# Performance work log

Measured on AMD Instinct MI355X. Metric: run time of the kernel, lower is better.

The kernel has to match this reference:

```python
import jax, jax.numpy as jnp
import numpy as np

B, IN_C, OUT_C, K, Z_DIM = 32, 128, 128, 3, 512
H, W, STRIDE = 56, 56, 1


def setup_inputs() -> dict:
    key = jax.random.key(0)
    k1, k2, k3 = jax.random.split(key, 3)
    x = jax.random.normal(k1, (B, IN_C, H, W), dtype=jnp.float32)
    z = jax.random.normal(k2, (B, Z_DIM), dtype=jnp.float32)
    # nn.Linear(z_dim, out_c*in_c*k*k): weight [out_f, in_f], bias [out_f]
    out_f = OUT_C * IN_C * K * K
    W_head = jax.random.normal(k3, (out_f, Z_DIM), dtype=jnp.float32) * (1.0 / np.sqrt(Z_DIM))
    b_head = jnp.zeros((out_f,), dtype=jnp.float32)
    return {"x": x, "z": z, "W_head": W_head, "b_head": b_head}


def reference(x, z, W_head, b_head):
    b = x.shape[0]
    # hypernetwork head: per-sample conv weights
    w = z @ W_head.T + b_head                       # [B, out_c*in_c*k*k]
    w = w.reshape(b, OUT_C, IN_C, K, K)             # [B, O, I, K, K]

    pad = K // 2

    def conv_one(xi, wi):
        # xi: [I, H, W], wi: [O, I, K, K] -> [O, H', W']
        out = jax.lax.conv_general_dilated(
            xi[None],                                # [1, I, H, W]
            wi,
            window_strides=(STRIDE, STRIDE),
            padding=[(pad, pad), (pad, pad)],
            dimension_numbers=("NCHW", "OIHW", "NCHW"),
        )
        return out[0]

    return jax.vmap(conv_one)(x, w)                 # [B, O, H', W']
```

## Files before the change

### kernel.cpp

```cpp
#include <hip/hip_runtime.h>
#include <hip/hip_bf16.h>
#include <stdint.h>

#define BB 32
#define IC 128
#define OC 128
#define HH 56
#define WW 56
#define ZD 512
#define NRS 9
#define OI (OC*IC)
#define WROWS (OI*NRS)
#define WDIM 58

typedef float  f32x4  __attribute__((ext_vector_type(4)));
typedef short  bf16x8 __attribute__((ext_vector_type(8)));

static __device__ __forceinline__ short f2bf(float f) {
    uint32_t u = __float_as_uint(f);
    uint32_t r = (u + 0x7fffu + ((u >> 16) & 1u)) >> 16;
    return (short)r;
}
static __device__ __forceinline__ short f2bf_hw(float f) {
    __hip_bfloat16 h = __float2bfloat16(f);
    return *reinterpret_cast<short*>(&h);
}

__global__ __launch_bounds__(256) void head_kernel(
    const float* __restrict__ Wh, const float* __restrict__ z,
    const float* __restrict__ bh, short* __restrict__ wout)
{
    __shared__ __align__(16) char Zl[32 * 1024];
    const int tid = threadIdx.x;

    {
        const int b = tid >> 3, ks = (tid & 7) * 64;
        const float* zp = z + (size_t)b * ZD + ks;
        const int bx = (b & 7) << 4;
        #pragma unroll
        for (int j8 = 0; j8 < 8; ++j8) {
            f32x4 v0 = *(const f32x4*)(zp + j8 * 8);
            f32x4 v1 = *(const f32x4*)(zp + j8 * 8 + 4);
            bf16x8 pk;
            pk[0] = f2bf_hw(v0.x); pk[1] = f2bf_hw(v0.y);
            pk[2] = f2bf_hw(v0.z); pk[3] = f2bf_hw(v0.w);
            pk[4] = f2bf_hw(v1.x); pk[5] = f2bf_hw(v1.y);
            pk[6] = f2bf_hw(v1.z); pk[7] = f2bf_hw(v1.w);
            *(bf16x8*)(Zl + b * 1024 + ((ks * 2 + j8 * 16) ^ bx)) = pk;
        }
    }
    __syncthreads();

    const int lane = tid & 63;
    const int wv   = tid >> 6;
    const int rl   = lane & 15;
    const int kq   = lane >> 4;
    const int rowg = blockIdx.x * 64 + wv * 16 + rl;
    const float* wp = Wh + (size_t)rowg * ZD + kq * 8;
    const int zxor = (rl & 7) << 4;

    f32x4 acc0 = {0.f, 0.f, 0.f, 0.f}, acc1 = {0.f, 0.f, 0.f, 0.f};
    #pragma unroll 4
    for (int kb = 0; kb < 16; ++kb) {
        f32x4 w0 = *(const f32x4*)(wp + kb * 32);
        f32x4 w1 = *(const f32x4*)(wp + kb * 32 + 4);
        bf16x8 bw;
        bw[0] = f2bf_hw(w0.x); bw[1] = f2bf_hw(w0.y);
        bw[2] = f2bf_hw(w0.z); bw[3] = f2bf_hw(w0.w);
        bw[4] = f2bf_hw(w1.x); bw[5] = f2bf_hw(w1.y);
        bw[6] = f2bf_hw(w1.z); bw[7] = f2bf_hw(w1.w);
        const int koff = (kb * 64 + kq * 16) ^ zxor;
        bf16x8 a0 = *(const bf16x8*)(Zl + rl * 1024 + koff);
        bf16x8 a1 = *(const bf16x8*)(Zl + (16 + rl) * 1024 + koff);
        acc0 = __builtin_amdgcn_mfma_f32_16x16x32_bf16(a0, bw, acc0, 0, 0, 0);
        acc1 = __builtin_amdgcn_mfma_f32_16x16x32_bf16(a1, bw, acc1, 0, 0, 0);
    }

    const float bias = bh[rowg];
    const int oi = rowg / 9, rs = rowg - oi * 9;
    const size_t outb = (size_t)rs * OI + oi;
    #pragma unroll
    for (int r = 0; r < 4; ++r) {
        const int b0 = kq * 4 + r;
        wout[(size_t)b0 * WROWS + outb]        = f2bf(acc0[r] + bias);
        wout[(size_t)(16 + b0) * WROWS + outb] = f2bf(acc1[r] + bias);
    }
}

__global__ __launch_bounds__(256) void transpose_kernel(
    const float* __restrict__ x, short* __restrict__ xt)
{
    const int h = blockIdx.x;
    const int b = blockIdx.y;
    const int w = threadIdx.x & 63;
    const int yq = threadIdx.x >> 6;
    if (w >= WW) return;
    const float* xp = x + (size_t)b * IC * HH * WW + h * WW + w;
    short* op = xt + (((size_t)(b * HH + h)) * WW + w) * IC;
    #pragma unroll
    for (int q = 0; q < 4; ++q) {
        int ic = yq * 4 + q;
        bf16x8 pk;
        #pragma unroll
        for (int j = 0; j < 8; ++j) {
            float v = xp[(size_t)(ic * 8 + j) * (HH * WW)];
            pk[j] = f2bf(v);
        }
        *(bf16x8*)(op + ic * 8) = pk;
    }
}

__global__ __launch_bounds__(256) void conv_kernel(
    const short* __restrict__ wbf,
    const short* __restrict__ xt,
    float* __restrict__ out)
{
    __shared__ __align__(16) char Xl[3 * WDIM * 256];
    __shared__ __align__(16) char Wl[128 * 256];
    const int tid  = threadIdx.x;
    const int lane = tid & 63;
    const int wv   = tid >> 6;
    const int h = blockIdx.x;
    const int b = blockIdx.y;

    #pragma unroll
    for (int q = 0; q < 11; ++q) {
        int idx = tid + q * 256;
        if (idx < 3 * WDIM * 16) ((f32x4*)Xl)[idx] = (f32x4){0.f, 0.f, 0.f, 0.f};
    }
    __syncthreads();

    for (int r = 0; r < 3; ++r) {
        int hin = h + r - 1;
        if (hin < 0 || hin >= HH) continue;
        const char* src = (const char*)(xt + ((size_t)(b * HH + hin)) * WW * IC);
        char* dstbase = Xl + (r * WDIM + 1) * 256;
        for (int it = wv; it < 14; it += 4) {
            int c = it * 64 + lane;
            int u = r * WDIM + 1 + (c >> 4);
            int soff = (c * 16) ^ ((u & 7) << 4);
            __builtin_amdgcn_global_load_lds(
                (const __attribute__((address_space(1))) uint32_t*)(src + soff),
                (__attribute__((address_space(3))) uint32_t*)(dstbase + it * 1024),
                16, 0, 0);
        }
    }

    f32x4 acc[2][4];
    #pragma unroll
    for (int a = 0; a < 2; ++a)
        #pragma unroll
        for (int p = 0; p < 4; ++p) acc[a][p] = (f32x4){0.f, 0.f, 0.f, 0.f};

    const int axor = (lane & 7) << 4;
    int kkoff[4];
    #pragma unroll
    for (int kk = 0; kk < 4; ++kk) kkoff[kk] = kk * 64 + ((lane >> 4) << 4);

    for (int rs = 0; rs < 9; ++rs) {
        __syncthreads();
        const char* wsrc = (const char*)(wbf + ((size_t)b * NRS + rs) * OI);
        for (int it = wv; it < 32; it += 4) {
            int c = it * 64 + lane;
            int soff = (c * 16) ^ (((c >> 4) & 7) << 4);
            __builtin_amdgcn_global_load_lds(
                (const __attribute__((address_space(1))) uint32_t*)(wsrc + soff),
                (__attribute__((address_space(3))) uint32_t*)(Wl + it * 1024),
                16, 0, 0);
        }
        __syncthreads();

        const int r = rs / 3, s = rs - 3 * (rs / 3);
        int ubase[4], bswz[4];
        #pragma unroll
        for (int pf = 0; pf < 4; ++pf) {
            int p = pf * 16 + (lane & 15);
            int pc = p > 55 ? 55 : p;
            int uu = r * WDIM + pc + s;
            ubase[pf] = uu * 256;
            bswz[pf] = (uu & 7) << 4;
        }
        #pragma unroll
        for (int kk = 0; kk < 4; ++kk) {
            bf16x8 a0 = *(const bf16x8*)(Wl + (wv * 32 + (lane & 15)) * 256 +
                                         (kkoff[kk] ^ axor));
            bf16x8 a1 = *(const bf16x8*)(Wl + (wv * 32 + 16 + (lane & 15)) * 256 +
                                         (kkoff[kk] ^ axor));
            #pragma unroll
            for (int pf = 0; pf < 4; ++pf) {
                bf16x8 bv = *(const bf16x8*)(Xl + ubase[pf] + (kkoff[kk] ^ bswz[pf]));
                acc[0][pf] = __builtin_amdgcn_mfma_f32_16x16x32_bf16(a0, bv, acc[0][pf], 0, 0, 0);
                acc[1][pf] = __builtin_amdgcn_mfma_f32_16x16x32_bf16(a1, bv, acc[1][pf], 0, 0, 0);
            }
        }
    }

    const int pcol = lane & 15;
    const int rowq = lane >> 4;
    #pragma unroll
    for (int a = 0; a < 2; ++a) {
        int o0 = wv * 32 + a * 16 + rowq * 4;
        #pragma unroll
        for (int pf = 0; pf < 4; ++pf) {
            int p = pf * 16 + pcol;
            if (p < WW) {
                #pragma unroll
                for (int reg = 0; reg < 4; ++reg) {
                    out[(((size_t)b * OC + (o0 + reg)) * HH + h) * WW + p] = acc[a][pf][reg];
                }
            }
        }
    }
}

extern "C" void kernel_launch(void* const* d_in, const int* in_sizes, int n_in,
                              void* d_out, int out_size, void* d_ws, size_t ws_size,
                              hipStream_t stream) {
    const float* x  = (const float*)d_in[0];
    const float* z  = (const float*)d_in[1];
    const float* Wh = (const float*)d_in[2];
    const float* bh = (const float*)d_in[3];
    float* out = (float*)d_out;

    short* wbf = (short*)d_ws;
    short* xt  = (short*)((char*)d_ws + (size_t)BB * NRS * OI * 2);

    head_kernel<<<dim3(WROWS / 64), 256, 0, stream>>>(Wh, z, bh, wbf);
    transpose_kernel<<<dim3(HH, BB), 256, 0, stream>>>(x, xt);
    conv_kernel<<<dim3(HH, BB), 256, 0, stream>>>(wbf, xt, out);
}
```

Before: 172.8 us.

## Double-buffer hypernet head weights through LDS with async global-to-LDS loads

The head GEMM kernel now streams W_head tiles into a double-buffered LDS region using global_load_lds, prefetching the next K-slice while computing the current one, and each block handles 128 rows instead of 64 (two row fragments per wave). This targets the latency-bound direct global loads of the 75MB fp32 weight matrix, which dominate the head kernel. It adds a barrier per K-step and more LDS per block, which may reduce occupancy.

```diff
diff --git a/kernel.cpp b/kernel.cpp
--- a/kernel.cpp
+++ b/kernel.cpp
@@ -31,7 +31,10 @@
     const float* __restrict__ bh, short* __restrict__ wout)
 {
     __shared__ __align__(16) char Zl[32 * 1024];
-    const int tid = threadIdx.x;
+    __shared__ __align__(16) char Wl[2 * 16384];
+    const int tid  = threadIdx.x;
+    const int lane = tid & 63;
+    const int wv   = tid >> 6;
 
     {
         const int b = tid >> 3, ks = (tid & 7) * 64;
@@ -49,42 +52,75 @@
             *(bf16x8*)(Zl + b * 1024 + ((ks * 2 + j8 * 16) ^ bx)) = pk;
         }
     }
+
+    const int lrow = wv * 8 + (lane >> 3);
+    const char* wsrc0 = (const char*)Wh
+        + ((size_t)(blockIdx.x * 128 + lrow)) * (ZD * 4)
+        + (((lane & 7) * 16) ^ (((lane >> 3) & 7) << 4));
+
+    #define STAGE_W(buf, kb)                                                     \
+        _Pragma("unroll")                                                        \
+        for (int rnd = 0; rnd < 4; ++rnd) {                                      \
+            __builtin_amdgcn_global_load_lds(                                    \
+                (const __attribute__((address_space(1))) uint32_t*)              \
+                    (wsrc0 + (size_t)rnd * 32 * (ZD * 4) + (kb) * 128),          \
+                (__attribute__((address_space(3))) uint32_t*)                    \
+                    (Wl + (buf) * 16384 + rnd * 4096 + wv * 1024),               \
+                16, 0, 0);                                                       \
+        }
+
+    STAGE_W(0, 0);
     __syncthreads();
 
-    const int lane = tid & 63;
-    const int wv   = tid >> 6;
-    const int rl   = lane & 15;
-    const int kq   = lane >> 4;
-    const int rowg = blockIdx.x * 64 + wv * 16 + rl;
-    const float* wp = Wh + (size_t)rowg * ZD + kq * 8;
+    const int rl = lane & 15;
+    const int kq = lane >> 4;
     const int zxor = (rl & 7) << 4;
 
-    f32x4 acc0 = {0.f, 0.f, 0.f, 0.f}, acc1 = {0.f, 0.f, 0.f, 0.f};
-    #pragma unroll 4
+    f32x4 acc[2][2];
+    #pragma unroll
+    for (int rf = 0; rf < 2; ++rf)
+        #pragma unroll
+        for (int bt = 0; bt < 2; ++bt) acc[rf][bt] = (f32x4){0.f, 0.f, 0.f, 0.f};
+
     for (int kb = 0; kb < 16; ++kb) {
-        f32x4 w0 = *(const f32x4*)(wp + kb * 32);
-        f32x4 w1 = *(const f32x4*)(wp + kb * 32 + 4);
-        bf16x8 bw;
-        bw[0] = f2bf_hw(w0.x); bw[1] = f2bf_hw(w0.y);
-        bw[2] = f2bf_hw(w0.z); bw[3] = f2bf_hw(w0.w);
-        bw[4] = f2bf_hw(w1.x); bw[5] = f2bf_hw(w1.y);
-        bw[6] = f2bf_hw(w1.z); bw[7] = f2bf_hw(w1.w);
+        const int cur = kb & 1;
+        if (kb < 15) STAGE_W(cur ^ 1, kb + 1);
+
         const int koff = (kb * 64 + kq * 16) ^ zxor;
         bf16x8 a0 = *(const bf16x8*)(Zl + rl * 1024 + koff);
         bf16x8 a1 = *(const bf16x8*)(Zl + (16 + rl) * 1024 + koff);
-        acc0 = __builtin_amdgcn_mfma_f32_16x16x32_bf16(a0, bw, acc0, 0, 0, 0);
-        acc1 = __builtin_amdgcn_mfma_f32_16x16x32_bf16(a1, bw, acc1, 0, 0, 0);
-    }
-
-    const float bias = bh[rowg];
-    const int oi = rowg / 9, rs = rowg - oi * 9;
-    const size_t outb = (size_t)rs * OI + oi;
-    #pragma unroll
-    for (int r = 0; r < 4; ++r) {
-        const int b0 = kq * 4 + r;
-        wout[(size_t)b0 * WROWS + outb]        = f2bf(acc0[r] + bias);
-        wout[(size_t)(16 + b0) * WROWS + outb] = f2bf(acc1[r] + bias);
-    }
+
+        #pragma unroll
+        for (int rf = 0; rf < 2; ++rf) {
+            const int r = (2 * wv + rf) * 16 + rl;
+            const char* wb = Wl + cur * 16384 + r * 128;
+            f32x4 lo = *(const f32x4*)(wb + ((kq * 32) ^ zxor));
+            f32x4 hi = *(const f32x4*)(wb + ((kq * 32 + 16) ^ zxor));
+            bf16x8 bw;
+            bw[0] = f2bf_hw(lo.x); bw[1] = f2bf_hw(lo.y);
+            bw[2] = f2bf_hw(lo.z); bw[3] = f2bf_hw(lo.w);
+            bw[4] = f2bf_hw(hi.x); bw[5] = f2bf_hw(hi.y);
+            bw[6] = f2bf_hw(hi.z); bw[7] = f2bf_hw(hi.w);
+            acc[rf][0] = __builtin_amdgcn_mfma_f32_16x16x32_bf16(a0, bw, acc[rf][0], 0, 0, 0);
+            acc[rf][1] = __builtin_amdgcn_mfma_f32_16x16x32_bf16(a1, bw, acc[rf][1], 0, 0, 0);
+        }
+        __syncthreads();
+    }
+
+    #pragma unroll
+    for (int rf = 0; rf < 2; ++rf) {
+        const int rowg = blockIdx.x * 128 + (2 * wv + rf) * 16 + rl;
+        const float bias = bh[rowg];
+        const int oi = rowg / 9, rs = rowg - oi * 9;
+        const size_t outb = (size_t)rs * OI + oi;
+        #pragma unroll
+        for (int reg = 0; reg < 4; ++reg) {
+            const int b0 = kq * 4 + reg;
+            wout[(size_t)b0 * WROWS + outb]        = f2bf(acc[rf][0][reg] + bias);
+            wout[(size_t)(16 + b0) * WROWS + outb] = f2bf(acc[rf][1][reg] + bias);
+        }
+    }
+    #undef STAGE_W
 }
 
 __global__ __launch_bounds__(256) void transpose_kernel(
@@ -225,7 +261,7 @@
     short* wbf = (short*)d_ws;
     short* xt  = (short*)((char*)d_ws + (size_t)BB * NRS * OI * 2);
 
-    head_kernel<<<dim3(WROWS / 64), 256, 0, stream>>>(Wh, z, bh, wbf);
+    head_kernel<<<dim3(WROWS / 128), 256, 0, stream>>>(Wh, z, bh, wbf);
     transpose_kernel<<<dim3(HH, BB), 256, 0, stream>>>(x, xt);
     conv_kernel<<<dim3(HH, BB), 256, 0, stream>>>(wbf, xt, out);
 }
```

After: 176.5 us. 2.1% more time.

## Pipeline hypernet head weight loads through LDS and split scattered store into repack kernel

Applied to the files above, without the earlier changes.

The head kernel now uses 256 persistent blocks that each stream W_head rows through a triple-buffered LDS ring with async global-to-LDS loads and explicit vmcnt waits, replacing direct global loads. It writes the per-sample weights in natural row order instead of the strided (rs,oi) scatter. A new repack kernel adds the bias and transposes into the layout the conv kernel expects. The goal is to hide memory latency on the large W_head read and make the stores contiguous, at the cost of an extra kernel launch and an extra round trip of about 9 MB through memory.

```diff
diff --git a/kernel.cpp b/kernel.cpp
--- a/kernel.cpp
+++ b/kernel.cpp
@@ -25,13 +25,25 @@
     __hip_bfloat16 h = __float2bfloat16(f);
     return *reinterpret_cast<short*>(&h);
 }
+static __device__ __forceinline__ float bf2f(short s) {
+    uint32_t u = ((uint32_t)(uint16_t)s) << 16;
+    return __uint_as_float(u);
+}
+static __device__ __forceinline__ void gll16(const void* g, void* l) {
+    __builtin_amdgcn_global_load_lds(
+        (const __attribute__((address_space(1))) uint32_t*)g,
+        (__attribute__((address_space(3))) uint32_t*)l, 16, 0, 0);
+}
 
 __global__ __launch_bounds__(256) void head_kernel(
     const float* __restrict__ Wh, const float* __restrict__ z,
-    const float* __restrict__ bh, short* __restrict__ wout)
+    short* __restrict__ wnat)
 {
     __shared__ __align__(16) char Zl[32 * 1024];
-    const int tid = threadIdx.x;
+    __shared__ __align__(16) char Wl[4 * 3 * 8192];
+    const int tid  = threadIdx.x;
+    const int lane = tid & 63;
+    const int wv   = tid >> 6;
 
     {
         const int b = tid >> 3, ks = (tid & 7) * 64;
@@ -51,39 +63,118 @@
     }
     __syncthreads();
 
-    const int lane = tid & 63;
-    const int wv   = tid >> 6;
-    const int rl   = lane & 15;
-    const int kq   = lane >> 4;
-    const int rowg = blockIdx.x * 64 + wv * 16 + rl;
-    const float* wp = Wh + (size_t)rowg * ZD + kq * 8;
+    const int rl = lane & 15;
+    const int kq = lane >> 4;
     const int zxor = (rl & 7) << 4;
-
-    f32x4 acc0 = {0.f, 0.f, 0.f, 0.f}, acc1 = {0.f, 0.f, 0.f, 0.f};
-    #pragma unroll 4
-    for (int kb = 0; kb < 16; ++kb) {
-        f32x4 w0 = *(const f32x4*)(wp + kb * 32);
-        f32x4 w1 = *(const f32x4*)(wp + kb * 32 + 4);
-        bf16x8 bw;
-        bw[0] = f2bf_hw(w0.x); bw[1] = f2bf_hw(w0.y);
-        bw[2] = f2bf_hw(w0.z); bw[3] = f2bf_hw(w0.w);
-        bw[4] = f2bf_hw(w1.x); bw[5] = f2bf_hw(w1.y);
-        bw[6] = f2bf_hw(w1.z); bw[7] = f2bf_hw(w1.w);
-        const int koff = (kb * 64 + kq * 16) ^ zxor;
-        bf16x8 a0 = *(const bf16x8*)(Zl + rl * 1024 + koff);
-        bf16x8 a1 = *(const bf16x8*)(Zl + (16 + rl) * 1024 + koff);
-        acc0 = __builtin_amdgcn_mfma_f32_16x16x32_bf16(a0, bw, acc0, 0, 0, 0);
-        acc1 = __builtin_amdgcn_mfma_f32_16x16x32_bf16(a1, bw, acc1, 0, 0, 0);
-    }
-
-    const float bias = bh[rowg];
-    const int oi = rowg / 9, rs = rowg - oi * 9;
-    const size_t outb = (size_t)rs * OI + oi;
-    #pragma unroll
-    for (int r = 0; r < 4; ++r) {
-        const int b0 = kq * 4 + r;
-        wout[(size_t)b0 * WROWS + outb]        = f2bf(acc0[r] + bias);
-        wout[(size_t)(16 + b0) * WROWS + outb] = f2bf(acc1[r] + bias);
+    const int q  = lane >> 5;
+
+    uint32_t O[4];
+    #pragma unroll
+    for (int j = 0; j < 4; ++j)
+        O[j] = j * 4096 + q * 2048 +
+               (((lane & 31) * 16) ^ (((2 * j + q) & 7) << 4));
+
+    const char* WB = (const char*)Wh +
+        (size_t)(blockIdx.x * 576 + wv * 16) * (ZD * 4);
+    char* WLb = Wl + wv * 24576;
+
+    #define STAGE(gg, ss, buf)                                                  \
+        {                                                                       \
+            const char* sb_ = WB + (size_t)(gg) * 131072 + (ss) * 512;          \
+            char* db_ = WLb + (buf) * 8192;                                     \
+            _Pragma("unroll")                                                   \
+            for (int i_ = 0; i_ < 8; ++i_)                                      \
+                gll16(sb_ + (i_ >> 2) * 16384 + O[i_ & 3], db_ + i_ * 1024);    \
+        }
+
+    STAGE(0, 0, 0);
+    STAGE(0, 1, 1);
+
+    int bufc = 0;
+    for (int g = 0; g < 9; ++g) {
+        f32x4 acc0 = {0.f, 0.f, 0.f, 0.f}, acc1 = {0.f, 0.f, 0.f, 0.f};
+        #pragma unroll
+        for (int s = 0; s < 4; ++s) {
+            if (s == 0) {
+                if (g) { asm volatile("s_waitcnt vmcnt(16)" ::: "memory"); }
+                else   { asm volatile("s_waitcnt vmcnt(8)"  ::: "memory"); }
+            } else if (s == 3) {
+                if (g == 8) { asm volatile("s_waitcnt vmcnt(0)" ::: "memory"); }
+                else        { asm volatile("s_waitcnt vmcnt(8)" ::: "memory"); }
+            } else {
+                asm volatile("s_waitcnt vmcnt(8)" ::: "memory");
+            }
+            __builtin_amdgcn_sched_barrier(0);
+
+            const char* cb = WLb + bufc * 8192;
+            #pragma unroll
+            for (int j = 0; j < 4; ++j) {
+                const int kb = s * 4 + j;
+                const int koff = (kb * 64 + kq * 16) ^ zxor;
+                bf16x8 a0 = *(const bf16x8*)(Zl + rl * 1024 + koff);
+                bf16x8 a1 = *(const bf16x8*)(Zl + (16 + rl) * 1024 + koff);
+                f32x4 lo = *(const f32x4*)(cb + rl * 512 + ((j * 128 + kq * 32) ^ zxor));
+                f32x4 hi = *(const f32x4*)(cb + rl * 512 + ((j * 128 + kq * 32 + 16) ^ zxor));
+                bf16x8 bw;
+                bw[0] = f2bf_hw(lo.x); bw[1] = f2bf_hw(lo.y);
+                bw[2] = f2bf_hw(lo.z); bw[3] = f2bf_hw(lo.w);
+                bw[4] = f2bf_hw(hi.x); bw[5] = f2bf_hw(hi.y);
+                bw[6] = f2bf_hw(hi.z); bw[7] = f2bf_hw(hi.w);
+                acc0 = __builtin_amdgcn_mfma_f32_16x16x32_bf16(a0, bw, acc0, 0, 0, 0);
+                acc1 = __builtin_amdgcn_mfma_f32_16x16x32_bf16(a1, bw, acc1, 0, 0, 0);
+            }
+
+            if (s == 3) {
+                const int rowg = blockIdx.x * 576 + g * 64 + wv * 16 + rl;
+                #pragma unroll
+                for (int reg = 0; reg < 4; ++reg) {
+                    const int b0 = kq * 4 + reg;
+                    wnat[(size_t)b0 * WROWS + rowg]        = f2bf(acc0[reg]);
+                    wnat[(size_t)(16 + b0) * WROWS + rowg] = f2bf(acc1[reg]);
+                }
+            }
+
+            {
+                const int su = 4 * g + s + 2;
+                if (su < 36) {
+                    const int sbuf = (bufc + 2) % 3;
+                    const int gg = g + (s >= 2 ? 1 : 0);
+                    const int ss = (s + 2) & 3;
+                    STAGE(gg, ss, sbuf);
+                }
+            }
+            bufc = (bufc == 2) ? 0 : bufc + 1;
+        }
+    }
+    #undef STAGE
+}
+
+__global__ __launch_bounds__(256) void repack_kernel(
+    const short* __restrict__ wnat, const float* __restrict__ bh,
+    short* __restrict__ wbf)
+{
+    const int b = blockIdx.y;
+    const int oi0 = blockIdx.x * 2048 + threadIdx.x * 8;
+    const short* src = wnat + (size_t)b * WROWS + (size_t)oi0 * 9;
+    const float* bp  = bh + (size_t)oi0 * 9;
+
+    bf16x8 in[9];
+    #pragma unroll
+    for (int j = 0; j < 9; ++j) in[j] = *(const bf16x8*)(src + j * 8);
+    f32x4 bv[18];
+    #pragma unroll
+    for (int m = 0; m < 18; ++m) bv[m] = *(const f32x4*)(bp + m * 4);
+
+    #pragma unroll
+    for (int rs = 0; rs < 9; ++rs) {
+        bf16x8 o;
+        #pragma unroll
+        for (int jj = 0; jj < 8; ++jj) {
+            const int e = jj * 9 + rs;
+            float v = bf2f(in[e >> 3][e & 7]) + bv[e >> 2][e & 3];
+            o[jj] = f2bf(v);
+        }
+        *(bf16x8*)(wbf + ((size_t)(b * 9 + rs)) * OI + oi0) = o;
     }
 }
 
@@ -139,10 +230,7 @@
             int c = it * 64 + lane;
             int u = r * WDIM + 1 + (c >> 4);
             int soff = (c * 16) ^ ((u & 7) << 4);
-            __builtin_amdgcn_global_load_lds(
-                (const __attribute__((address_space(1))) uint32_t*)(src + soff),
-                (__attribute__((address_space(3))) uint32_t*)(dstbase + it * 1024),
-                16, 0, 0);
+            gll16(src + soff, dstbase + it * 1024);
         }
     }
 
@@ -163,10 +251,7 @@
         for (int it = wv; it < 32; it += 4) {
             int c = it * 64 + lane;
             int soff = (c * 16) ^ (((c >> 4) & 7) << 4);
-            __builtin_amdgcn_global_load_lds(
-                (const __attribute__((address_space(1))) uint32_t*)(wsrc + soff),
-                (__attribute__((address_space(3))) uint32_t*)(Wl + it * 1024),
-                16, 0, 0);
+            gll16(wsrc + soff, Wl + it * 1024);
         }
         __syncthreads();
 
@@ -222,10 +307,12 @@
     const float* bh = (const float*)d_in[3];
     float* out = (float*)d_out;
 
-    short* wbf = (short*)d_ws;
-    short* xt  = (short*)((char*)d_ws + (size_t)BB * NRS * OI * 2);
-
-    head_kernel<<<dim3(WROWS / 64), 256, 0, stream>>>(Wh, z, bh, wbf);
+    short* wnat = (short*)d_ws;
+    short* wbf  = (short*)((char*)d_ws + 9437184);
+    short* xt   = (short*)((char*)d_ws + 18874368);
+
+    head_kernel<<<dim3(256), 256, 0, stream>>>(Wh, z, wnat);
+    repack_kernel<<<dim3(8, 32), 256, 0, stream>>>(wnat, bh, wbf);
     transpose_kernel<<<dim3(HH, BB), 256, 0, stream>>>(x, xt);
     conv_kernel<<<dim3(HH, BB), 256, 0, stream>>>(wbf, xt, out);
 }
```

After: 164.5 us. -4.8%, faster.
